# Performance work log

Hardware: AMD Instinct MI355X
Metric: run time of the kernel (lower is better)

## Reference

```python
import jax, jax.numpy as jnp
import numpy as np

B, T, D = 4, 2048, 1024  # batch, seq_len, dec_dim_in == dim_proj_QK == dim_proj_V == dec_dim_out


def setup_inputs() -> dict:
    key = jax.random.key(0)
    ks = jax.random.split(key, 9)
    s = 1.0 / np.sqrt(D)  # torch Linear default init scale
    return {
        "x": jax.random.normal(ks[0], (B, T, D), dtype=jnp.float32),
        "Wq": jax.random.uniform(ks[1], (D, D), jnp.float32, -s, s),
        "bq": jax.random.uniform(ks[2], (D,), jnp.float32, -s, s),
        "Wk": jax.random.uniform(ks[3], (D, D), jnp.float32, -s, s),
        "bk": jax.random.uniform(ks[4], (D,), jnp.float32, -s, s),
        "Wv": jax.random.uniform(ks[5], (D, D), jnp.float32, -s, s),
        "bv": jax.random.uniform(ks[6], (D,), jnp.float32, -s, s),
        "Wh": jax.random.uniform(ks[7], (D, D), jnp.float32, -s, s),
        "bh": jax.random.uniform(ks[8], (D,), jnp.float32, -s, s),
    }


def reference(x, Wq, bq, Wk, bk, Wv, bv, Wh, bh):
    Q = x @ Wq + bq                      # [B, T, Dqk]
    K = x @ Wk + bk                      # [B, T, Dqk]
    V = x @ Wv + bv                      # [B, T, Dv]
    scale = 1.0 / jnp.sqrt(jnp.asarray(K.shape[-1], x.dtype))
    scores = jnp.einsum("btd,bsd->bts", Q, K) * scale  # [B, T, T]
    t = K.shape[1]
    causal = jnp.triu(jnp.ones((t, t), dtype=bool), k=1)  # True above diagonal
    scores = jnp.where(causal[None, :, :], -jnp.inf, scores)
    attn = jax.nn.softmax(scores, axis=-1)
    # dropout is identity in eval mode (reference baseline)
    out = jnp.einsum("bts,bsd->btd", attn, V)  # [B, T, Dv]
    return out @ Wh + bh
```

## Files before the change

kernel.cpp:

```cpp
#include <hip/hip_runtime.h>


typedef __attribute__((ext_vector_type(8)))  short short8;
typedef __attribute__((ext_vector_type(4)))  float f4;
typedef __attribute__((ext_vector_type(8)))  unsigned short us8;

#define BM 128
#define BN 128
#define BK 64

__device__ inline unsigned short f2bf(float f) {
    union { float f; unsigned u; } c; c.f = f;
    unsigned u = c.u;
    return (unsigned short)((u + 0x7fffu + ((u >> 16) & 1u)) >> 16);
}
__device__ inline float bf2f(unsigned short u) {
    union { unsigned u; float f; } c; c.u = ((unsigned)u) << 16;
    return c.f;
}
__device__ inline void gload16(const void* g, void* l) {
    __builtin_amdgcn_global_load_lds(
        (const __attribute__((address_space(1))) void*)g,
        (__attribute__((address_space(3))) void*)l,
        16, 0, 0);
}

__global__ __launch_bounds__(256)
void gemm_bt(const unsigned short* __restrict__ A,
             const unsigned short* __restrict__ Bt,
             void* __restrict__ C,
             const float* __restrict__ bias,
             int M, int N, int K, int lda, int ldb, int ldc,
             long sA, long sB, long sC,
             float scale, int flags,
             unsigned short* __restrict__ C2, long sC2, int Tv, int vsplit,
             const float* __restrict__ rowscale)
{
    const int b = blockIdx.z;
    A  += (long)b * sA;
    Bt += (long)b * sB;
    if (flags & 32) rowscale += (long)b * M;

    int by = blockIdx.y;
    if (flags & 8) by = gridDim.y - 1 - by;
    const int m0 = by * BM;
    const int n0 = blockIdx.x * BN;

    if ((flags & 2) && n0 > m0 + (BM - 1)) return;

    int kend = K;
    if (flags & 4) { int ke = m0 + BM; kend = ke < K ? ke : K; }
    const int numK = kend / BK;

    __shared__ unsigned short As[BM * BK];
    __shared__ unsigned short Bs[BN * BK];

    const int tid  = threadIdx.x;
    const int lane = tid & 63;
    const int wave = tid >> 6;
    const int wm   = wave & 1;
    const int wn   = wave >> 1;
    const int lrow = lane & 15;
    const int quad = lane >> 4;

    f4 acc[4][4];
#pragma unroll
    for (int i = 0; i < 4; ++i)
#pragma unroll
        for (int j = 0; j < 4; ++j) acc[i][j] = (f4)0.0f;

    const int srow = tid >> 3;
    const int gco  = ((tid & 7) ^ (srow & 7)) << 3;
    const int rdsl = (lrow & 7);

    for (int kt = 0; kt < numK; ++kt) {
        const int k0 = kt * BK;
#pragma unroll
        for (int d = 0; d < 4; ++d) {
            const int row = d * 32 + srow;
            const unsigned short* ga = A  + (long)(m0 + row) * lda + k0 + gco;
            const unsigned short* gb = Bt + (long)(n0 + row) * ldb + k0 + gco;
            const int ldsoff = (d * 256 + wave * 64) * 16;
            gload16(ga, (char*)As + ldsoff);
            gload16(gb, (char*)Bs + ldsoff);
        }
        __syncthreads();

#pragma unroll
        for (int ks = 0; ks < 2; ++ks) {
            const int slot = ((ks * 4 + quad) ^ rdsl) << 3;
            short8 af[4], bfr[4];
#pragma unroll
            for (int i = 0; i < 4; ++i) {
                af[i]  = *(const short8*)(As + (wm * 64 + i * 16 + lrow) * BK + slot);
                bfr[i] = *(const short8*)(Bs + (wn * 64 + i * 16 + lrow) * BK + slot);
            }
#pragma unroll
            for (int i = 0; i < 4; ++i)
#pragma unroll
                for (int j = 0; j < 4; ++j)
                    acc[i][j] = __builtin_amdgcn_mfma_f32_16x16x32_bf16(
                        af[i], bfr[j], acc[i][j], 0, 0, 0);
        }
        __syncthreads();
    }

    const int row0 = m0 + wm * 64 + quad * 4;
    const int col0 = n0 + wn * 64 + lrow;

    float bj[4];
#pragma unroll
    for (int j = 0; j < 4; ++j) bj[j] = bias ? bias[col0 + j * 16] : 0.0f;

    if ((flags & 16) && n0 >= vsplit) {
        const int bidx  = m0 >> 11;
        const int tloc0 = (m0 & 2047) + wm * 64 + quad * 4;
#pragma unroll
        for (int j = 0; j < 4; ++j) {
            const int d = col0 + j * 16 - vsplit;
            unsigned short* base = C2 + (long)bidx * sC2 + (long)d * Tv;
#pragma unroll
            for (int i = 0; i < 4; ++i) {
                const int tt = tloc0 + i * 16;
                unsigned long long pk = 0;
#pragma unroll
                for (int r = 0; r < 4; ++r) {
                    float v = acc[i][j][r] * scale + bj[j];
                    pk |= (unsigned long long)f2bf(v) << (16 * r);
                }
                *(unsigned long long*)(base + tt) = pk;
            }
        }
        return;
    }

    const bool obf = flags & 1;
    unsigned short* Cb = (unsigned short*)C;
    float*          Cf = (float*)C;
    const long cbase = (long)b * sC;

#pragma unroll
    for (int i = 0; i < 4; ++i) {
#pragma unroll
        for (int j = 0; j < 4; ++j) {
            const int col = col0 + j * 16;
#pragma unroll
            for (int r = 0; r < 4; ++r) {
                const int row = row0 + i * 16 + r;
                float v = acc[i][j][r] * scale;
                if (flags & 64) { v = __expf(v); if (col > row) v = 0.0f; }
                if (flags & 32) v *= rowscale[row];
                v += bj[j];
                const long off = cbase + (long)row * ldc + col;
                if (obf) Cb[off] = f2bf(v);
                else     Cf[off] = v;
            }
        }
    }
}

__global__ void rowsum(const unsigned short* __restrict__ P,
                       float* __restrict__ invl, int T)
{
    const int t = blockIdx.x;
    const long rowoff = ((long)blockIdx.y * T + t) * T;
    const int L = t + 1;
    const int tid = threadIdx.x;
    const int lane = tid & 63, wave = tid >> 6;
    __shared__ float red[4];

    us8 raw = *(const us8*)(P + rowoff + tid * 8);
    const int i0 = tid * 8;
    float sum = 0.0f;
#pragma unroll
    for (int k = 0; k < 8; ++k)
        if (i0 + k < L) sum += bf2f(raw[k]);
    for (int o = 32; o > 0; o >>= 1) sum += __shfl_down(sum, o);
    if (lane == 0) red[wave] = sum;
    __syncthreads();
    if (tid == 0) {
        sum = red[0] + red[1] + red[2] + red[3];
        invl[(long)blockIdx.y * T + t] = 1.0f / sum;
    }
}

__global__ void gemv_bhh(const unsigned short* __restrict__ Wht,
                         const float* __restrict__ bv,
                         const float* __restrict__ bh,
                         float* __restrict__ bhh)
{
    const int m = blockIdx.x;
    const int tid = threadIdx.x;
    const int lane = tid & 63, wave = tid >> 6;
    __shared__ float red[4];
    const unsigned short* row = Wht + (long)m * 1024;
    float s = 0.0f;
#pragma unroll
    for (int k = 0; k < 4; ++k) {
        const int idx = tid * 4 + k;
        s += bf2f(row[idx]) * bv[idx];
    }
    for (int o = 32; o > 0; o >>= 1) s += __shfl_down(s, o);
    if (lane == 0) red[wave] = s;
    __syncthreads();
    if (tid == 0) bhh[m] = red[0] + red[1] + red[2] + red[3] + bh[m];
}

__global__ void prep(const float* __restrict__ x,
                     const float* __restrict__ Wq, const float* __restrict__ Wk,
                     const float* __restrict__ Wv, const float* __restrict__ Wh,
                     const float* __restrict__ bq, const float* __restrict__ bk,
                     unsigned short* __restrict__ Xbf,
                     unsigned short* __restrict__ Wqkvt,
                     unsigned short* __restrict__ Wht,
                     unsigned short* __restrict__ Wvb,
                     float* __restrict__ bqkv)
{
    typedef __attribute__((ext_vector_type(4))) float f4v;
    __shared__ unsigned short tsh[32][33];
    const int bid = blockIdx.x;
    const int tid = threadIdx.x;

    if (bid < 8192) {
        const int i = bid * 256 + tid;
        f4v v = ((const f4v*)x)[i];
        unsigned long long p = (unsigned long long)f2bf(v.x)
                             | ((unsigned long long)f2bf(v.y) << 16)
                             | ((unsigned long long)f2bf(v.z) << 32)
                             | ((unsigned long long)f2bf(v.w) << 48);
        ((unsigned long long*)Xbf)[i] = p;
    } else if (bid < 9216) {
        const int i = (bid - 8192) * 256 + tid;
        f4v v = ((const f4v*)Wv)[i];
        unsigned long long p = (unsigned long long)f2bf(v.x)
                             | ((unsigned long long)f2bf(v.y) << 16)
                             | ((unsigned long long)f2bf(v.z) << 32)
                             | ((unsigned long long)f2bf(v.w) << 48);
        ((unsigned long long*)Wvb)[i] = p;
    } else if (bid < 12288) {
        const int wi = bid - 9216;
        const int w = wi >> 10, tile = wi & 1023;
        const float* src = (w == 0) ? Wq : (w == 1) ? Wk : Wh;
        unsigned short* dst = (w == 0) ? Wqkvt : (w == 1) ? (Wqkvt + 1024 * 1024) : Wht;
        const int c0 = (tile & 31) * 32, r0 = (tile >> 5) * 32;
        const int xx = tid & 31, yy = tid >> 5;
        for (int i = yy; i < 32; i += 8)
            tsh[i][xx] = f2bf(src[(long)(r0 + i) * 1024 + c0 + xx]);
        __syncthreads();
        for (int i = yy; i < 32; i += 8)
            dst[(long)(c0 + i) * 1024 + r0 + xx] = tsh[xx][i];
    } else {
        const int i = (bid - 12288) * 256 + tid;
        if (i < 1024) { bqkv[i] = bq[i]; bqkv[1024 + i] = bk[i]; bqkv[2048 + i] = 0.0f; }
    }
}

extern "C" void kernel_launch(void* const* d_in, const int* in_sizes, int n_in,
                              void* d_out, int out_size, void* d_ws, size_t ws_size,
                              hipStream_t stream)
{
    const float* x  = (const float*)d_in[0];
    const float* Wq = (const float*)d_in[1];
    const float* bq = (const float*)d_in[2];
    const float* Wk = (const float*)d_in[3];
    const float* bk = (const float*)d_in[4];
    const float* Wv = (const float*)d_in[5];
    const float* bv = (const float*)d_in[6];
    const float* Wh = (const float*)d_in[7];
    const float* bh = (const float*)d_in[8];
    float* out = (float*)d_out;

    const int  Bb = 4, T = 2048, Dm = 1024;
    const long BT = (long)Bb * T;

    unsigned short* ws = (unsigned short*)d_ws;
    size_t o = 0;
    unsigned short* Xbf   = ws + o; o += (size_t)BT * Dm;
    unsigned short* Wqkvt = ws + o; o += (size_t)3 * Dm * Dm;
    unsigned short* Wht   = ws + o; o += (size_t)Dm * Dm;
    unsigned short* Wvb   = ws + o; o += (size_t)Dm * Dm;
    float* bqkv = (float*)(ws + o); o += (size_t)3 * Dm * 2;
    float* bhh  = (float*)(ws + o); o += (size_t)Dm * 2;
    unsigned short* QKV   = ws + o; o += (size_t)BT * 3 * Dm;
    unsigned short* Vt    = ws + o; o += (size_t)BT * Dm;
    unsigned short* Pp    = ws + o; o += (size_t)Bb * T * T;
    float* invlb = (float*)(ws + o); o += (size_t)BT * 2;

    const dim3 blk(256);
    const long sRow3 = (long)T * 3 * Dm;

    prep<<<12289, blk, 0, stream>>>(x, Wq, Wk, Wv, Wh, bq, bk,
                                    Xbf, Wqkvt, Wht, Wvb, bqkv);

    gemm_bt<<<dim3(Dm / BN, Dm / BM, 1), blk, 0, stream>>>(
        Wht, Wvb, Wqkvt + 2 * Dm * Dm, nullptr, Dm, Dm, Dm, Dm, Dm, Dm,
        0, 0, 0, 1.0f, 1, nullptr, 0, 0, 0, nullptr);

    gemv_bhh<<<Dm, blk, 0, stream>>>(Wht, bv, bh, bhh);

    gemm_bt<<<dim3(3 * Dm / BN, BT / BM, 1), blk, 0, stream>>>(
        Xbf, Wqkvt, QKV, bqkv, (int)BT, 3 * Dm, Dm, Dm, Dm, 3 * Dm,
        0, 0, 0, 1.0f, 1 | 16, Vt, (long)Dm * T, T, 2 * Dm, nullptr);

    gemm_bt<<<dim3(T / BN, T / BM, Bb), blk, 0, stream>>>(
        QKV, QKV + Dm, Pp, nullptr, T, T, Dm, 3 * Dm, 3 * Dm, T,
        sRow3, sRow3, (long)T * T, 1.0f / 32.0f, 1 | 2 | 8 | 64,
        nullptr, 0, 0, 0, nullptr);

    rowsum<<<dim3(T, Bb), blk, 0, stream>>>(Pp, invlb, T);

    gemm_bt<<<dim3(Dm / BN, T / BM, Bb), blk, 0, stream>>>(
        Pp, Vt, out, bhh, T, Dm, T, T, T, Dm,
        (long)T * T, (long)Dm * T, (long)T * Dm, 1.0f, 4 | 8 | 32,
        nullptr, 0, 0, 0, invlb);
}
```

Measured before the change: 318.0 us.

## Fuse row-sum into score GEMM, split-K the PV GEMM, template flags

Computes the softmax row sums inside the score GEMM epilogue with shuffles and atomics, which removes the separate rowsum kernel and its reread of P. The PV GEMM is split along K for row blocks past 1024 so the long causal rows use more blocks, with a second pass adding the partials. Flags become template parameters so each variant is compiled without runtime branches. The cost is atomics, an extra fp32 partial buffer and a combine kernel. Row sums are now taken from fp32 values before bf16 rounding, so they differ slightly from the rounded P they normalise.

Measured after the change: 309.2 us. -2.8%, faster.

```diff
diff --git a/kernel.cpp b/kernel.cpp
--- a/kernel.cpp
+++ b/kernel.cpp
@@ -8,6 +8,16 @@
 #define BM 128
 #define BN 128
 #define BK 64
+
+#define F_OBF    1
+#define F_SKIP   2
+#define F_KLIM   4
+#define F_REVY   8
+#define F_VSPL   16
+#define F_RSCL   32
+#define F_EXP    64
+#define F_RSUM   128
+#define F_SPLITK 256
 
 __device__ inline unsigned short f2bf(float f) {
     union { float f; unsigned u; } c; c.f = f;
@@ -25,6 +35,7 @@
         16, 0, 0);
 }
 
+template<int FLAGS>
 __global__ __launch_bounds__(256)
 void gemm_bt(const unsigned short* __restrict__ A,
              const unsigned short* __restrict__ Bt,
@@ -32,25 +43,39 @@
              const float* __restrict__ bias,
              int M, int N, int K, int lda, int ldb, int ldc,
              long sA, long sB, long sC,
-             float scale, int flags,
+             float scale,
              unsigned short* __restrict__ C2, long sC2, int Tv, int vsplit,
-             const float* __restrict__ rowscale)
+             float* __restrict__ rowsums)
 {
     const int b = blockIdx.z;
     A  += (long)b * sA;
     Bt += (long)b * sB;
-    if (flags & 32) rowscale += (long)b * M;
+    if (FLAGS & (F_RSCL | F_RSUM)) rowsums += (long)b * M;
 
     int by = blockIdx.y;
-    if (flags & 8) by = gridDim.y - 1 - by;
+    if (FLAGS & F_REVY) by = gridDim.y - 1 - by;
     const int m0 = by * BM;
-    const int n0 = blockIdx.x * BN;
-
-    if ((flags & 2) && n0 > m0 + (BM - 1)) return;
+
+    int n0, split = 0;
+    if (FLAGS & F_SPLITK) {
+        const int nbx = N / BN;
+        n0 = (blockIdx.x % nbx) * BN;
+        split = blockIdx.x / nbx;
+        if (split && m0 < 1024) return;
+    } else {
+        n0 = blockIdx.x * BN;
+    }
+
+    if ((FLAGS & F_SKIP) && n0 > m0 + (BM - 1)) return;
 
     int kend = K;
-    if (flags & 4) { int ke = m0 + BM; kend = ke < K ? ke : K; }
-    const int numK = kend / BK;
+    if (FLAGS & F_KLIM) { int ke = m0 + BM; kend = ke < K ? ke : K; }
+    int kt0 = 0;
+    if (FLAGS & F_SPLITK) {
+        if (split == 0) { if (kend > 1024) kend = 1024; }
+        else            { kt0 = 1024 / BK; }
+    }
+    const int kt1 = kend / BK;
 
     __shared__ unsigned short As[BM * BK];
     __shared__ unsigned short Bs[BN * BK];
@@ -73,7 +98,7 @@
     const int gco  = ((tid & 7) ^ (srow & 7)) << 3;
     const int rdsl = (lrow & 7);
 
-    for (int kt = 0; kt < numK; ++kt) {
+    for (int kt = kt0; kt < kt1; ++kt) {
         const int k0 = kt * BK;
 #pragma unroll
         for (int d = 0; d < 4; ++d) {
@@ -112,7 +137,7 @@
 #pragma unroll
     for (int j = 0; j < 4; ++j) bj[j] = bias ? bias[col0 + j * 16] : 0.0f;
 
-    if ((flags & 16) && n0 >= vsplit) {
+    if ((FLAGS & F_VSPL) && n0 >= vsplit) {
         const int bidx  = m0 >> 11;
         const int tloc0 = (m0 & 2047) + wm * 64 + quad * 4;
 #pragma unroll
@@ -134,9 +159,23 @@
         return;
     }
 
-    const bool obf = flags & 1;
+    float inv[16];
+    if (FLAGS & F_RSCL) {
+#pragma unroll
+        for (int i = 0; i < 4; ++i)
+#pragma unroll
+            for (int r = 0; r < 4; ++r)
+                inv[i * 4 + r] = 1.0f / rowsums[row0 + i * 16 + r];
+    }
+
+    float rs[16];
+    if (FLAGS & F_RSUM) {
+#pragma unroll
+        for (int k = 0; k < 16; ++k) rs[k] = 0.0f;
+    }
+
     unsigned short* Cb = (unsigned short*)C;
-    float*          Cf = (float*)C;
+    float*          Cf = ((FLAGS & F_SPLITK) && split) ? (float*)C2 : (float*)C;
     const long cbase = (long)b * sC;
 
 #pragma unroll
@@ -148,40 +187,44 @@
             for (int r = 0; r < 4; ++r) {
                 const int row = row0 + i * 16 + r;
                 float v = acc[i][j][r] * scale;
-                if (flags & 64) { v = __expf(v); if (col > row) v = 0.0f; }
-                if (flags & 32) v *= rowscale[row];
-                v += bj[j];
+                if (FLAGS & F_EXP) { v = __expf(v); if (col > row) v = 0.0f; }
+                if (FLAGS & F_RSUM) rs[i * 4 + r] += v;
+                if (FLAGS & F_RSCL) v *= inv[i * 4 + r];
+                if (!((FLAGS & F_SPLITK) && split)) v += bj[j];
                 const long off = cbase + (long)row * ldc + col;
-                if (obf) Cb[off] = f2bf(v);
-                else     Cf[off] = v;
+                if (FLAGS & F_OBF) Cb[off] = f2bf(v);
+                else               Cf[off] = v;
             }
         }
     }
-}
-
-__global__ void rowsum(const unsigned short* __restrict__ P,
-                       float* __restrict__ invl, int T)
-{
-    const int t = blockIdx.x;
-    const long rowoff = ((long)blockIdx.y * T + t) * T;
-    const int L = t + 1;
-    const int tid = threadIdx.x;
-    const int lane = tid & 63, wave = tid >> 6;
-    __shared__ float red[4];
-
-    us8 raw = *(const us8*)(P + rowoff + tid * 8);
-    const int i0 = tid * 8;
-    float sum = 0.0f;
-#pragma unroll
-    for (int k = 0; k < 8; ++k)
-        if (i0 + k < L) sum += bf2f(raw[k]);
-    for (int o = 32; o > 0; o >>= 1) sum += __shfl_down(sum, o);
-    if (lane == 0) red[wave] = sum;
-    __syncthreads();
-    if (tid == 0) {
-        sum = red[0] + red[1] + red[2] + red[3];
-        invl[(long)blockIdx.y * T + t] = 1.0f / sum;
-    }
+
+    if (FLAGS & F_RSUM) {
+#pragma unroll
+        for (int k = 0; k < 16; ++k) {
+            rs[k] += __shfl_xor(rs[k], 1);
+            rs[k] += __shfl_xor(rs[k], 2);
+            rs[k] += __shfl_xor(rs[k], 4);
+            rs[k] += __shfl_xor(rs[k], 8);
+        }
+        if (lrow == 0) {
+#pragma unroll
+            for (int i = 0; i < 4; ++i)
+#pragma unroll
+                for (int r = 0; r < 4; ++r)
+                    atomicAdd(&rowsums[row0 + i * 16 + r], rs[i * 4 + r]);
+        }
+    }
+}
+
+__global__ void combine_upper(float* __restrict__ out,
+                              const float* __restrict__ part)
+{
+    const long base = ((long)blockIdx.y * 2048 + 1024) * 1024 / 4;
+    const long i = base + blockIdx.x * 256 + threadIdx.x;
+    f4 a = ((f4*)out)[i];
+    f4 bb = ((const f4*)part)[i];
+    a.x += bb.x; a.y += bb.y; a.z += bb.z; a.w += bb.w;
+    ((f4*)out)[i] = a;
 }
 
 __global__ void gemv_bhh(const unsigned short* __restrict__ Wht,
@@ -216,14 +259,13 @@
                      unsigned short* __restrict__ Wvb,
                      float* __restrict__ bqkv)
 {
-    typedef __attribute__((ext_vector_type(4))) float f4v;
     __shared__ unsigned short tsh[32][33];
     const int bid = blockIdx.x;
     const int tid = threadIdx.x;
 
     if (bid < 8192) {
         const int i = bid * 256 + tid;
-        f4v v = ((const f4v*)x)[i];
+        f4 v = ((const f4*)x)[i];
         unsigned long long p = (unsigned long long)f2bf(v.x)
                              | ((unsigned long long)f2bf(v.y) << 16)
                              | ((unsigned long long)f2bf(v.z) << 32)
@@ -231,7 +273,7 @@
         ((unsigned long long*)Xbf)[i] = p;
     } else if (bid < 9216) {
         const int i = (bid - 8192) * 256 + tid;
-        f4v v = ((const f4v*)Wv)[i];
+        f4 v = ((const f4*)Wv)[i];
         unsigned long long p = (unsigned long long)f2bf(v.x)
                              | ((unsigned long long)f2bf(v.y) << 16)
                              | ((unsigned long long)f2bf(v.z) << 32)
@@ -281,36 +323,41 @@
     unsigned short* Wvb   = ws + o; o += (size_t)Dm * Dm;
     float* bqkv = (float*)(ws + o); o += (size_t)3 * Dm * 2;
     float* bhh  = (float*)(ws + o); o += (size_t)Dm * 2;
+    float* sums = (float*)(ws + o); o += (size_t)BT * 2;
     unsigned short* QKV   = ws + o; o += (size_t)BT * 3 * Dm;
     unsigned short* Vt    = ws + o; o += (size_t)BT * Dm;
     unsigned short* Pp    = ws + o; o += (size_t)Bb * T * T;
-    float* invlb = (float*)(ws + o); o += (size_t)BT * 2;
+    float* part = (float*)(ws + o);
 
     const dim3 blk(256);
     const long sRow3 = (long)T * 3 * Dm;
 
+    hipMemsetAsync(sums, 0, (size_t)BT * sizeof(float), stream);
+
     prep<<<12289, blk, 0, stream>>>(x, Wq, Wk, Wv, Wh, bq, bk,
                                     Xbf, Wqkvt, Wht, Wvb, bqkv);
 
-    gemm_bt<<<dim3(Dm / BN, Dm / BM, 1), blk, 0, stream>>>(
+    gemm_bt<F_OBF><<<dim3(Dm / BN, Dm / BM, 1), blk, 0, stream>>>(
         Wht, Wvb, Wqkvt + 2 * Dm * Dm, nullptr, Dm, Dm, Dm, Dm, Dm, Dm,
-        0, 0, 0, 1.0f, 1, nullptr, 0, 0, 0, nullptr);
+        0, 0, 0, 1.0f, nullptr, 0, 0, 0, nullptr);
 
     gemv_bhh<<<Dm, blk, 0, stream>>>(Wht, bv, bh, bhh);
 
-    gemm_bt<<<dim3(3 * Dm / BN, BT / BM, 1), blk, 0, stream>>>(
+    gemm_bt<F_OBF | F_VSPL><<<dim3(3 * Dm / BN, BT / BM, 1), blk, 0, stream>>>(
         Xbf, Wqkvt, QKV, bqkv, (int)BT, 3 * Dm, Dm, Dm, Dm, 3 * Dm,
-        0, 0, 0, 1.0f, 1 | 16, Vt, (long)Dm * T, T, 2 * Dm, nullptr);
-
-    gemm_bt<<<dim3(T / BN, T / BM, Bb), blk, 0, stream>>>(
+        0, 0, 0, 1.0f, Vt, (long)Dm * T, T, 2 * Dm, nullptr);
+
+    gemm_bt<F_OBF | F_SKIP | F_REVY | F_EXP | F_RSUM>
+        <<<dim3(T / BN, T / BM, Bb), blk, 0, stream>>>(
         QKV, QKV + Dm, Pp, nullptr, T, T, Dm, 3 * Dm, 3 * Dm, T,
-        sRow3, sRow3, (long)T * T, 1.0f / 32.0f, 1 | 2 | 8 | 64,
-        nullptr, 0, 0, 0, nullptr);
-
-    rowsum<<<dim3(T, Bb), blk, 0, stream>>>(Pp, invlb, T);
-
-    gemm_bt<<<dim3(Dm / BN, T / BM, Bb), blk, 0, stream>>>(
+        sRow3, sRow3, (long)T * T, 1.0f / 32.0f,
+        nullptr, 0, 0, 0, sums);
+
+    gemm_bt<F_KLIM | F_REVY | F_RSCL | F_SPLITK>
+        <<<dim3(2 * Dm / BN, T / BM, Bb), blk, 0, stream>>>(
         Pp, Vt, out, bhh, T, Dm, T, T, T, Dm,
-        (long)T * T, (long)Dm * T, (long)T * Dm, 1.0f, 4 | 8 | 32,
-        nullptr, 0, 0, 0, invlb);
-}
+        (long)T * T, (long)Dm * T, (long)T * Dm, 1.0f,
+        (unsigned short*)part, 0, 0, 0, sums);
+
+    combine_upper<<<dim3(1024, Bb), blk, 0, stream>>>(out, part);
+}
```
